# Kernel tuning notes

Hardware: AMD Instinct MI355X
Metric: run time of the kernel (lower is better)

## Reference

```python
import jax, jax.numpy as jnp
import numpy as np

T = 8          # number of adapter tasks
H = 1024       # hidden_size
I = 4096       # intermediate_size (bert dense input)
D = H // 16    # adapter bottleneck (reduction_factor=16)
B, S = 8, 512
EPS = 1e-12    # BERT LayerNorm eps


def _layernorm(x, g, b):
    mu = jnp.mean(x, axis=-1, keepdims=True)
    var = jnp.mean(jnp.square(x - mu), axis=-1, keepdims=True)
    return (x - mu) * jax.lax.rsqrt(var + EPS) * g + b


def setup_inputs() -> dict:
    key = jax.random.key(0)
    ks = jax.random.split(key, 14)
    std = 0.02
    inp = {
        "hidden_states": jax.random.normal(ks[0], (B, S, I), jnp.float32),
        "input_tensor": jax.random.normal(ks[1], (B, S, H), jnp.float32),
        "dense_w": jax.random.normal(ks[2], (H, I), jnp.float32) * std,
        "dense_b": jnp.zeros((H,), jnp.float32),
        "ln_g": jnp.ones((H,), jnp.float32),
        "ln_b": jnp.zeros((H,), jnp.float32),
        "down_w": jax.random.normal(ks[3], (T, D, H), jnp.float32) * std,
        "down_b": jnp.zeros((T, D), jnp.float32),
        "up_w": jax.random.normal(ks[4], (T, H, D), jnp.float32) * std,
        "up_b": jnp.zeros((T, H), jnp.float32),
        "key_w": jax.random.normal(ks[5], (H, H), jnp.float32) * std,
        "key_b": jnp.zeros((H,), jnp.float32),
        "query_w": jax.random.normal(ks[6], (H, H), jnp.float32) * std,
        "query_b": jnp.zeros((H,), jnp.float32),
        # value init: near-zero with identity diagonal
        "value_w": jnp.full((H, H), 1e-6, jnp.float32).at[jnp.arange(H), jnp.arange(H)].set(1.0),
    }
    return inp


def reference(hidden_states, input_tensor, dense_w, dense_b, ln_g, ln_b,
              down_w, down_b, up_w, up_b, key_w, key_b, query_w, query_b, value_w):
    # dense: [B,S,I] @ [H,I]^T -> [B,S,H]   (dropout = identity in eval)
    h = jnp.einsum('bsi,hi->bsh', hidden_states, dense_w) + dense_b
    prenorm = input_tensor + h
    adapter_in = _layernorm(prenorm, ln_g, ln_b)
    # batched per-task adapters: down-project, relu, up-project -> [T,B,S,H]
    down = jax.nn.relu(jnp.einsum('bsh,tdh->tbsd', adapter_in, down_w)
                       + down_b[:, None, None, :])
    adapter_out = jnp.einsum('tbsd,thd->tbsh', down, up_w) + up_b[:, None, None, :]
    # fusion attention over task axis T
    key = jnp.einsum('tbsh,kh->tbsk', adapter_out, key_w) + key_b
    value = jnp.einsum('tbsh,vh->tbsv', adapter_out + h[None], value_w)
    query = jnp.einsum('bsh,qh->bsq', prenorm, query_w) + query_b
    scores = jnp.sum(query[None] * key, axis=-1, keepdims=True)  # [T,B,S,1]
    probs = jax.nn.softmax(scores, axis=0)
    fusion = jnp.sum(probs * value, axis=0)                       # [B,S,H]
    return _layernorm(input_tensor + fusion, ln_g, ln_b)
```

## Files before the change

kernel.cpp:

```cpp
#include <hip/hip_runtime.h>
#include <cstdint>
#include <cstddef>

typedef float   f32x4 __attribute__((ext_vector_type(4)));
typedef _Float16 f16x8 __attribute__((ext_vector_type(8)));
typedef _Float16 f16x4 __attribute__((ext_vector_type(4)));

#define TOK  4096
#define HID  1024
#define IDIM 4096

#define GLDS16(gp, lp) __builtin_amdgcn_global_load_lds(                      \
    (const __attribute__((address_space(1))) void*)(gp),                      \
    (__attribute__((address_space(3))) void*)(lp), 16, 0, 0)


__global__ __launch_bounds__(256, 4) void gemm_dense(
    const _Float16* __restrict__ A, const _Float16* __restrict__ B,
    int K, int Kchunk, float* __restrict__ part)
{
    __shared__ _Float16 lA[2][4096];
    __shared__ _Float16 lB[2][4096];
    const int tid  = threadIdx.x;
    const int lane = tid & 63;
    const int wave = tid >> 6;
    const int m0   = blockIdx.x * 128;
    const int n0   = blockIdx.y * 128;
    const int kz0  = blockIdx.z * Kchunk;
    const int wM   = (wave & 1) * 64;
    const int wN   = (wave >> 1) * 64;

    const int srow = lane >> 2;
    const int scol = ((lane & 3) ^ ((lane >> 3) & 3)) * 8;
    const _Float16* gA0 = A + (size_t)(m0 + wave * 32 + srow) * K + kz0 + scol;
    const _Float16* gA1 = gA0 + (size_t)16 * K;
    const _Float16* gB0 = B + (size_t)(n0 + wave * 32 + srow) * K + kz0 + scol;
    const _Float16* gB1 = gB0 + (size_t)16 * K;
    const int soff = wave * 1024;

    f32x4 acc[4][4] = {};
    const int fr  = lane & 15;
    const int khr = lane >> 4;
    const int kxo = (khr ^ ((fr >> 1) & 3)) * 8;

    GLDS16(gA0, &lA[0][soff]);
    GLDS16(gA1, &lA[0][soff + 512]);
    GLDS16(gB0, &lB[0][soff]);
    GLDS16(gB1, &lB[0][soff + 512]);
    __syncthreads();

    int cur = 0;
    for (int k = 0; k < Kchunk; k += 32) {
        if (k + 32 < Kchunk) {
            const int nb = cur ^ 1;
            GLDS16(gA0 + k + 32, &lA[nb][soff]);
            GLDS16(gA1 + k + 32, &lA[nb][soff + 512]);
            GLDS16(gB0 + k + 32, &lB[nb][soff]);
            GLDS16(gB1 + k + 32, &lB[nb][soff + 512]);
        }
        f16x8 afr[4], bfr[4];
#pragma unroll
        for (int mi = 0; mi < 4; ++mi)
            afr[mi] = *(const f16x8*)(&lA[cur][(wM + mi * 16 + fr) * 32 + kxo]);
#pragma unroll
        for (int ni = 0; ni < 4; ++ni)
            bfr[ni] = *(const f16x8*)(&lB[cur][(wN + ni * 16 + fr) * 32 + kxo]);
#pragma unroll
        for (int mi = 0; mi < 4; ++mi)
#pragma unroll
            for (int ni = 0; ni < 4; ++ni)
                acc[mi][ni] = __builtin_amdgcn_mfma_f32_16x16x32_f16(
                    afr[mi], bfr[ni], acc[mi][ni], 0, 0, 0);
        __syncthreads();
        cur ^= 1;
    }

    float* dst = part + (size_t)blockIdx.z * TOK * HID;
    const int cn = lane & 15;
    const int rq = (lane >> 4) * 4;
#pragma unroll
    for (int mi = 0; mi < 4; ++mi)
#pragma unroll
        for (int r = 0; r < 4; ++r) {
            const int m = m0 + wM + mi * 16 + rq + r;
#pragma unroll
            for (int ni = 0; ni < 4; ++ni) {
                const int n = n0 + wN + ni * 16 + cn;
                dst[(size_t)m * HID + n] = acc[mi][ni][r];
            }
        }
}

template <int MODE>
__global__ __launch_bounds__(1024, 4) void gemm_w32(
    const _Float16* __restrict__ Ah, const _Float16* __restrict__ B,
    int K, int Ncols,
    float* __restrict__ outF, _Float16* __restrict__ outH,
    const float* __restrict__ bias, const float* __restrict__ addv,
    const float* __restrict__ probs, const float* __restrict__ upb,
    const _Float16* __restrict__ A2, const _Float16* __restrict__ B2,
    _Float16* __restrict__ outH2)
{
    __shared__ _Float16 lA[2][4096];
    __shared__ _Float16 lB[2][4096];
    const int tid  = threadIdx.x;
    const int lane = tid & 63;
    const int wave = tid >> 6;
    const int m0   = blockIdx.x * 128;
    int n0, half = 0;
    const _Float16* Ap = Ah;
    const _Float16* Bp = B;
    if constexpr (MODE == 5) {
        half = blockIdx.y >> 2;
        n0 = (blockIdx.y & 3) * 128;
        if (half) { Ap = A2; Bp = B2; }
    } else {
        n0 = blockIdx.y * 128;
    }
    const int wM = (wave & 3) * 32;
    const int wN = (wave >> 2) * 32;

    f32x4 acc[2][2] = {};

    const int i8   = wave & 7;
    const int srow = lane >> 2;
    const int scol = ((lane & 3) ^ ((lane >> 3) & 3)) * 8;
    const _Float16* gsrc = ((wave < 8)
        ? Ap + (size_t)(m0 + i8 * 16 + srow) * K
        : Bp + (size_t)(n0 + i8 * 16 + srow) * K) + scol;
    _Float16* ldst = ((wave < 8) ? &lA[0][0] : &lB[0][0]) + i8 * 512;

    const int fr  = lane & 15;
    const int khr = lane >> 4;
    const int kxo = (khr ^ ((fr >> 1) & 3)) * 8;

    GLDS16(gsrc, ldst);
    __syncthreads();

    int cur = 0;
    for (int k0 = 0; k0 < K; k0 += 32) {
        if (k0 + 32 < K)
            GLDS16(gsrc + k0 + 32, ldst + (cur ^ 1) * 4096);
        f16x8 afr[2], bfr[2];
#pragma unroll
        for (int mi = 0; mi < 2; ++mi)
            afr[mi] = *(const f16x8*)(&lA[cur][(wM + mi * 16 + fr) * 32 + kxo]);
#pragma unroll
        for (int ni = 0; ni < 2; ++ni)
            bfr[ni] = *(const f16x8*)(&lB[cur][(wN + ni * 16 + fr) * 32 + kxo]);
#pragma unroll
        for (int mi = 0; mi < 2; ++mi)
#pragma unroll
            for (int ni = 0; ni < 2; ++ni)
                acc[mi][ni] = __builtin_amdgcn_mfma_f32_16x16x32_f16(
                    afr[mi], bfr[ni], acc[mi][ni], 0, 0, 0);
        __syncthreads();
        cur ^= 1;
    }

    const int cn = lane & 15;
    const int rq = (lane >> 4) * 4;
#pragma unroll
    for (int mi = 0; mi < 2; ++mi)
#pragma unroll
        for (int r = 0; r < 4; ++r) {
            const int m = m0 + wM + mi * 16 + rq + r;
#pragma unroll
            for (int ni = 0; ni < 2; ++ni) {
                const int n = n0 + wN + ni * 16 + cn;
                const float v = acc[mi][ni][r];
                if constexpr (MODE == 1) {
                    const float bb = bias ? bias[n] : 0.f;
                    outH[(size_t)m * Ncols + n] = (_Float16)(v + bb);
                } else if constexpr (MODE == 3) {
                    const size_t idx = (size_t)m * Ncols + n;
                    float s = v + addv[idx];
#pragma unroll
                    for (int t = 0; t < 8; ++t)
                        s += probs[(size_t)m * 8 + t] * upb[t * 1024 + n];
                    outH[idx] = (_Float16)s;
                } else if constexpr (MODE == 4) {
                    const size_t idx = (size_t)m * Ncols + n;
                    outF[idx] = v + addv[idx];
                } else {
                    const size_t idx = (size_t)m * 512 + n;
                    if (half == 0) {
                        const float y = v + bias[n];
                        outH[idx] = (_Float16)(y > 0.f ? y : 0.f);
                    } else {
                        outH2[idx] = (_Float16)v;
                    }
                }
            }
        }
}

__global__ __launch_bounds__(256) void ln_fused(
    const float* __restrict__ part, int sk,
    const float* __restrict__ dbias, const float* __restrict__ it,
    const float* __restrict__ gam, const float* __restrict__ bet,
    float* __restrict__ h_f32, _Float16* __restrict__ ai, _Float16* __restrict__ pn)
{
    const int n = blockIdx.x, tid = threadIdx.x;
    const int lane = tid & 63, wave = tid >> 6;
    const size_t base = (size_t)n * 1024 + tid * 4;
    f32x4 h = *(const f32x4*)(dbias + tid * 4);
    for (int z = 0; z < sk; ++z)
        h += *(const f32x4*)(part + (size_t)z * TOK * HID + base);
    *(f32x4*)(h_f32 + base) = h;
    f32x4 x = h + *(const f32x4*)(it + base);
    float s = x[0] + x[1] + x[2] + x[3];
    float q = x[0] * x[0] + x[1] * x[1] + x[2] * x[2] + x[3] * x[3];
#pragma unroll
    for (int off = 1; off < 64; off <<= 1) {
        s += __shfl_xor(s, off);
        q += __shfl_xor(q, off);
    }
    __shared__ float rs[4], rq[4];
    if (lane == 0) { rs[wave] = s; rq[wave] = q; }
    __syncthreads();
    s = rs[0] + rs[1] + rs[2] + rs[3];
    q = rq[0] + rq[1] + rq[2] + rq[3];
    const float mu = s * (1.f / 1024.f);
    const float var = q * (1.f / 1024.f) - mu * mu;
    const float rstd = rsqrtf(var + 1e-12f);
    f32x4 gv = *(const f32x4*)(gam + tid * 4);
    f32x4 bv = *(const f32x4*)(bet + tid * 4);
    f16x4 av, pv;
#pragma unroll
    for (int j = 0; j < 4; ++j) {
        const float y = (x[j] - mu) * rstd * gv[j] + bv[j];
        av[j] = (_Float16)y;
        pv[j] = (_Float16)x[j];
    }
    *(f16x4*)(ai + base) = av;
    *(f16x4*)(pn + base) = pv;
}

__global__ __launch_bounds__(256) void ln_out(
    const float* __restrict__ fuse, const float* __restrict__ gam,
    const float* __restrict__ bet, float* __restrict__ outp)
{
    const int n = blockIdx.x, tid = threadIdx.x;
    const int lane = tid & 63, wave = tid >> 6;
    const size_t base = (size_t)n * 1024 + tid * 4;
    f32x4 x = *(const f32x4*)(fuse + base);
    float s = x[0] + x[1] + x[2] + x[3];
    float q = x[0] * x[0] + x[1] * x[1] + x[2] * x[2] + x[3] * x[3];
#pragma unroll
    for (int off = 1; off < 64; off <<= 1) {
        s += __shfl_xor(s, off);
        q += __shfl_xor(q, off);
    }
    __shared__ float rs[4], rq[4];
    if (lane == 0) { rs[wave] = s; rq[wave] = q; }
    __syncthreads();
    s = rs[0] + rs[1] + rs[2] + rs[3];
    q = rq[0] + rq[1] + rq[2] + rq[3];
    const float mu = s * (1.f / 1024.f);
    const float var = q * (1.f / 1024.f) - mu * mu;
    const float rstd = rsqrtf(var + 1e-12f);
    f32x4 gv = *(const f32x4*)(gam + tid * 4);
    f32x4 bv = *(const f32x4*)(bet + tid * 4);
    f32x4 y;
#pragma unroll
    for (int j = 0; j < 4; ++j) y[j] = (x[j] - mu) * rstd * gv[j] + bv[j];
    *(f32x4*)(outp + base) = y;
}

__global__ __launch_bounds__(256) void scores_softmax(
    const _Float16* __restrict__ qk, const float* __restrict__ up_b,
    const _Float16* __restrict__ down, const _Float16* __restrict__ g,
    float* __restrict__ probs_out, _Float16* __restrict__ wdown)
{
    const int n = blockIdx.x, tid = threadIdx.x;
    const int lane = tid & 63, wave = tid >> 6;
    const _Float16* qkrow = qk + (size_t)n * 1024;
    float ub[8] = {};
#pragma unroll
    for (int j = 0; j < 4; ++j) {
        const int h = tid + j * 256;
        const float qkv = (float)qkrow[h];
#pragma unroll
        for (int t = 0; t < 8; ++t) ub[t] += qkv * up_b[t * 1024 + h];
    }
#pragma unroll
    for (int off = 1; off < 64; off <<= 1) {
#pragma unroll
        for (int t = 0; t < 8; ++t) ub[t] += __shfl_xor(ub[t], off);
    }
    __shared__ float red[4][9];
    __shared__ float sd[8];
    __shared__ float pl[8];
    if (lane == 0) {
#pragma unroll
        for (int t = 0; t < 8; ++t) red[wave][t] = ub[t];
    }
    const int c0 = tid * 2;
    const size_t dbase = (size_t)n * 512;
    const float d0 = (float)down[dbase + c0];
    const float d1 = (float)down[dbase + c0 + 1];
    float pz = d0 * (float)g[dbase + c0] + d1 * (float)g[dbase + c0 + 1];
#pragma unroll
    for (int off = 1; off < 32; off <<= 1) pz += __shfl_xor(pz, off);
    if ((lane & 31) == 0) sd[wave * 2 + (lane >> 5)] = pz;
    __syncthreads();
    if (tid == 0) {
        float sc[8];
        float mx = -1e30f;
#pragma unroll
        for (int t = 0; t < 8; ++t) {
            sc[t] = sd[t] + red[0][t] + red[1][t] + red[2][t] + red[3][t];
            mx = fmaxf(mx, sc[t]);
        }
        float sum = 0.f;
#pragma unroll
        for (int t = 0; t < 8; ++t) { sc[t] = expf(sc[t] - mx); sum += sc[t]; }
        const float inv = 1.f / sum;
#pragma unroll
        for (int t = 0; t < 8; ++t) pl[t] = sc[t] * inv;
    }
    __syncthreads();
    const float pr = pl[c0 >> 6];
    wdown[dbase + c0]     = (_Float16)(pr * d0);
    wdown[dbase + c0 + 1] = (_Float16)(pr * d1);
    if (tid < 8) probs_out[(size_t)n * 8 + tid] = pl[tid];
}

__device__ inline void cvt_seg(const float* __restrict__ s, _Float16* __restrict__ d,
                               int n4, int gid, int gsz)
{
    for (int i = gid; i < n4; i += gsz) {
        f32x4 v = ((const f32x4*)s)[i];
        f16x4 o;
        o[0] = (_Float16)v[0]; o[1] = (_Float16)v[1];
        o[2] = (_Float16)v[2]; o[3] = (_Float16)v[3];
        ((f16x4*)d)[i] = o;
    }
}

__global__ __launch_bounds__(256) void convert4(
    const float* s0, _Float16* d0, int n0,
    const float* s1, _Float16* d1, int n1,
    const float* s2, _Float16* d2, int n2,
    const float* s3, _Float16* d3, int n3,
    float* bz)
{
    if (blockIdx.x == 0) {
        f32x4 z = {0.f, 0.f, 0.f, 0.f};
        *(f32x4*)(bz + threadIdx.x * 4) = z;
    }
    const int gid = blockIdx.x * 256 + threadIdx.x;
    const int gsz = gridDim.x * 256;
    cvt_seg(s0, d0, n0, gid, gsz);
    cvt_seg(s1, d1, n1, gid, gsz);
    cvt_seg(s2, d2, n2, gid, gsz);
    cvt_seg(s3, d3, n3, gid, gsz);
}

__global__ __launch_bounds__(256) void transpose_kw(
    const float* __restrict__ in, _Float16* __restrict__ outp,
    const float* __restrict__ rvec, float* __restrict__ rout)
{
    __shared__ float t[32][33];
    __shared__ float rpart[8][33];
    const int bx = blockIdx.x * 32;
    const int by = blockIdx.y * 32;
    const int tx = threadIdx.x & 31, ty = threadIdx.x >> 5;
#pragma unroll
    for (int j = 0; j < 32; j += 8)
        t[ty + j][tx] = in[(size_t)(by + ty + j) * 1024 + bx + tx];
    __syncthreads();
#pragma unroll
    for (int j = 0; j < 32; j += 8)
        outp[(size_t)(bx + ty + j) * 1024 + by + tx] = (_Float16)t[tx][ty + j];
    if (rvec) {
        float s = 0.f;
#pragma unroll
        for (int j = 0; j < 4; ++j) {
            const int k = ty * 4 + j;
            s += rvec[by + k] * t[k][tx];
        }
        rpart[ty][tx] = s;
        __syncthreads();
        if (ty == 0) {
            float v = rpart[0][tx];
#pragma unroll
            for (int r = 1; r < 8; ++r) v += rpart[r][tx];
            atomicAdd(rout + bx + tx, v);
        }
    }
}

__global__ __launch_bounds__(256) void reshape_up(
    const float* __restrict__ up_w, _Float16* __restrict__ upg,
    _Float16* __restrict__ upmix)
{
    const int i = blockIdx.x * 256 + threadIdx.x;
    const int d = i & 63;
    const int h = (i >> 6) & 1023;
    const int t = i >> 16;
    const float v = up_w[i];
    upg[(size_t)(t * 64 + d) * 1024 + h] = (_Float16)v;
    upmix[(size_t)h * 512 + t * 64 + d]  = (_Float16)v;
}

extern "C" void kernel_launch(void* const* d_in, const int* in_sizes, int n_in,
                              void* d_out, int out_size, void* d_ws, size_t ws_size,
                              hipStream_t stream)
{
    const float* hs      = (const float*)d_in[0];
    const float* it      = (const float*)d_in[1];
    const float* dense_w = (const float*)d_in[2];
    const float* dense_b = (const float*)d_in[3];
    const float* ln_g    = (const float*)d_in[4];
    const float* ln_b    = (const float*)d_in[5];
    const float* down_w  = (const float*)d_in[6];
    const float* down_b  = (const float*)d_in[7];
    const float* up_w    = (const float*)d_in[8];
    const float* up_b    = (const float*)d_in[9];
    const float* key_w   = (const float*)d_in[10];
    const float* key_b   = (const float*)d_in[11];
    const float* query_w = (const float*)d_in[12];
    const float* query_b = (const float*)d_in[13];
    const float* value_w = (const float*)d_in[14];
    float* outp = (float*)d_out;
    (void)in_sizes; (void)n_in; (void)out_size; (void)key_b;

    const size_t MiB = 1ull << 20;
    char* p = (char*)d_ws;
    _Float16* w_dense  = (_Float16*)p; p += 8 * MiB;
    _Float16* w_queryT = (_Float16*)p; p += 2 * MiB;
    _Float16* w_keyT   = (_Float16*)p; p += 2 * MiB;
    _Float16* w_value  = (_Float16*)p; p += 2 * MiB;
    _Float16* w_fuseT  = (_Float16*)p; p += 2 * MiB;
    _Float16* w_down   = (_Float16*)p; p += 1 * MiB;
    _Float16* w_upg    = (_Float16*)p; p += 1 * MiB;
    _Float16* w_upmix  = (_Float16*)p; p += 1 * MiB;
    float*    bfuse    = (float*)p;    p += 1 * MiB;
    float*    h_f32    = (float*)p;    p += 16 * MiB;
    _Float16* ai       = (_Float16*)p; p += 8 * MiB;
    _Float16* pn       = (_Float16*)p; p += 8 * MiB;
    _Float16* hs_h = (_Float16*)h_f32;
    char* rb = p;
    const int sk = (ws_size >= (size_t)(52 + 64) * MiB) ? 4 : 2;
    float*    part  = (float*)rb;
    _Float16* qk    = (_Float16*)(rb +  8 * MiB);
    _Float16* down  = (_Float16*)(rb + 16 * MiB);
    _Float16* g     = (_Float16*)(rb + 20 * MiB);
    _Float16* wdown = (_Float16*)(rb + 24 * MiB);
    float*    probs = (float*)(rb + 28 * MiB);
    float*    fuse  = (float*)rb;
    _Float16* mixed = ai;

    convert4<<<2048, 256, 0, stream>>>(hs, hs_h, TOK * IDIM / 4,
                                       dense_w, w_dense, HID * IDIM / 4,
                                       value_w, w_value, HID * HID / 4,
                                       down_w,  w_down,  512 * HID / 4,
                                       bfuse);
    transpose_kw<<<dim3(32, 32), 256, 0, stream>>>(key_w, w_keyT, query_b, bfuse);
    transpose_kw<<<dim3(32, 32), 256, 0, stream>>>(query_w, w_queryT, nullptr, nullptr);
    reshape_up<<<2048, 256, 0, stream>>>(up_w, w_upg, w_upmix);
    gemm_w32<1><<<dim3(8, 8), 1024, 0, stream>>>(
        w_keyT, w_queryT, HID, HID, nullptr, w_fuseT, nullptr, nullptr, nullptr,
        nullptr, nullptr, nullptr, nullptr);

    gemm_dense<<<dim3(32, 8, sk), 256, 0, stream>>>(hs_h, w_dense, IDIM, IDIM / sk, part);
    ln_fused<<<TOK, 256, 0, stream>>>(part, sk, dense_b, it, ln_g, ln_b, h_f32, ai, pn);
    gemm_w32<1><<<dim3(32, 8), 1024, 0, stream>>>(
        pn, w_fuseT, HID, HID, nullptr, qk, bfuse, nullptr, nullptr, nullptr,
        nullptr, nullptr, nullptr);
    gemm_w32<5><<<dim3(32, 8), 1024, 0, stream>>>(
        ai, w_down, HID, 512, nullptr, down, down_b, nullptr, nullptr, nullptr,
        qk, w_upg, g);
    scores_softmax<<<TOK, 256, 0, stream>>>(qk, up_b, down, g, probs, wdown);
    gemm_w32<3><<<dim3(32, 8), 1024, 0, stream>>>(
        wdown, w_upmix, 512, HID, nullptr, mixed, nullptr, h_f32, probs, up_b,
        nullptr, nullptr, nullptr);
    gemm_w32<4><<<dim3(32, 8), 1024, 0, stream>>>(
        mixed, w_value, HID, HID, fuse, nullptr, nullptr, it, nullptr, nullptr,
        nullptr, nullptr, nullptr);
    ln_out<<<TOK, 256, 0, stream>>>(fuse, ln_g, ln_b, outp);
}
```

Measured before the change: 345.2 us.

## Rework 128x128 GEMM tile to 4 waves with 64x64 per-wave subtiles

The secondary GEMM kernel moves from 16 waves, each computing 32x32, to 4 waves, each computing 64x64, on the same 128x128 block tile. Each wave now issues four global-to-LDS loads per stage instead of one. It also reads 4+4 fragments for 16 MFMAs, which raises the MFMA-to-LDS-read ratio and lowers barrier cost per FLOP. The MODE 3 epilogue hoists the per-row probs loads out of the column loop. The trade-off is more accumulator registers per thread and fewer waves to hide latency, since a 128x128 grid with 32x8 blocks yields only 256 blocks.

```diff
diff --git a/kernel.cpp b/kernel.cpp
--- a/kernel.cpp
+++ b/kernel.cpp
@@ -92,7 +92,7 @@
 }
 
 template <int MODE>
-__global__ __launch_bounds__(1024, 4) void gemm_w32(
+__global__ __launch_bounds__(256, 4) void gemm_tile(
     const _Float16* __restrict__ Ah, const _Float16* __restrict__ B,
     int K, int Ncols,
     float* __restrict__ outF, _Float16* __restrict__ outH,
@@ -117,41 +117,48 @@
     } else {
         n0 = blockIdx.y * 128;
     }
-    const int wM = (wave & 3) * 32;
-    const int wN = (wave >> 2) * 32;
-
-    f32x4 acc[2][2] = {};
-
-    const int i8   = wave & 7;
+    const int wM = (wave & 1) * 64;
+    const int wN = (wave >> 1) * 64;
+
     const int srow = lane >> 2;
     const int scol = ((lane & 3) ^ ((lane >> 3) & 3)) * 8;
-    const _Float16* gsrc = ((wave < 8)
-        ? Ap + (size_t)(m0 + i8 * 16 + srow) * K
-        : Bp + (size_t)(n0 + i8 * 16 + srow) * K) + scol;
-    _Float16* ldst = ((wave < 8) ? &lA[0][0] : &lB[0][0]) + i8 * 512;
-
+    const _Float16* gA0 = Ap + (size_t)(m0 + wave * 32 + srow) * K + scol;
+    const _Float16* gA1 = gA0 + (size_t)16 * K;
+    const _Float16* gB0 = Bp + (size_t)(n0 + wave * 32 + srow) * K + scol;
+    const _Float16* gB1 = gB0 + (size_t)16 * K;
+    const int soff = wave * 1024;
+
+    f32x4 acc[4][4] = {};
     const int fr  = lane & 15;
     const int khr = lane >> 4;
     const int kxo = (khr ^ ((fr >> 1) & 3)) * 8;
 
-    GLDS16(gsrc, ldst);
+    GLDS16(gA0, &lA[0][soff]);
+    GLDS16(gA1, &lA[0][soff + 512]);
+    GLDS16(gB0, &lB[0][soff]);
+    GLDS16(gB1, &lB[0][soff + 512]);
     __syncthreads();
 
     int cur = 0;
-    for (int k0 = 0; k0 < K; k0 += 32) {
-        if (k0 + 32 < K)
-            GLDS16(gsrc + k0 + 32, ldst + (cur ^ 1) * 4096);
-        f16x8 afr[2], bfr[2];
-#pragma unroll
-        for (int mi = 0; mi < 2; ++mi)
+    for (int k = 0; k < K; k += 32) {
+        if (k + 32 < K) {
+            const int nb = cur ^ 1;
+            GLDS16(gA0 + k + 32, &lA[nb][soff]);
+            GLDS16(gA1 + k + 32, &lA[nb][soff + 512]);
+            GLDS16(gB0 + k + 32, &lB[nb][soff]);
+            GLDS16(gB1 + k + 32, &lB[nb][soff + 512]);
+        }
+        f16x8 afr[4], bfr[4];
+#pragma unroll
+        for (int mi = 0; mi < 4; ++mi)
             afr[mi] = *(const f16x8*)(&lA[cur][(wM + mi * 16 + fr) * 32 + kxo]);
 #pragma unroll
-        for (int ni = 0; ni < 2; ++ni)
+        for (int ni = 0; ni < 4; ++ni)
             bfr[ni] = *(const f16x8*)(&lB[cur][(wN + ni * 16 + fr) * 32 + kxo]);
 #pragma unroll
-        for (int mi = 0; mi < 2; ++mi)
-#pragma unroll
-            for (int ni = 0; ni < 2; ++ni)
+        for (int mi = 0; mi < 4; ++mi)
+#pragma unroll
+            for (int ni = 0; ni < 4; ++ni)
                 acc[mi][ni] = __builtin_amdgcn_mfma_f32_16x16x32_f16(
                     afr[mi], bfr[ni], acc[mi][ni], 0, 0, 0);
         __syncthreads();
@@ -161,12 +168,17 @@
     const int cn = lane & 15;
     const int rq = (lane >> 4) * 4;
 #pragma unroll
-    for (int mi = 0; mi < 2; ++mi)
+    for (int mi = 0; mi < 4; ++mi)
 #pragma unroll
         for (int r = 0; r < 4; ++r) {
             const int m = m0 + wM + mi * 16 + rq + r;
-#pragma unroll
-            for (int ni = 0; ni < 2; ++ni) {
+            float pr8[8];
+            if constexpr (MODE == 3) {
+#pragma unroll
+                for (int t = 0; t < 8; ++t) pr8[t] = probs[(size_t)m * 8 + t];
+            }
+#pragma unroll
+            for (int ni = 0; ni < 4; ++ni) {
                 const int n = n0 + wN + ni * 16 + cn;
                 const float v = acc[mi][ni][r];
                 if constexpr (MODE == 1) {
@@ -177,13 +189,13 @@
                     float s = v + addv[idx];
 #pragma unroll
                     for (int t = 0; t < 8; ++t)
-                        s += probs[(size_t)m * 8 + t] * upb[t * 1024 + n];
+                        s += pr8[t] * upb[t * 1024 + n];
                     outH[idx] = (_Float16)s;
                 } else if constexpr (MODE == 4) {
                     const size_t idx = (size_t)m * Ncols + n;
                     outF[idx] = v + addv[idx];
                 } else {
-                    const size_t idx = (size_t)m * 512 + n;
+                    const size_t idx = (size_t)m * Ncols + n;
                     if (half == 0) {
                         const float y = v + bias[n];
                         outH[idx] = (_Float16)(y > 0.f ? y : 0.f);
@@ -461,23 +473,23 @@
     transpose_kw<<<dim3(32, 32), 256, 0, stream>>>(key_w, w_keyT, query_b, bfuse);
     transpose_kw<<<dim3(32, 32), 256, 0, stream>>>(query_w, w_queryT, nullptr, nullptr);
     reshape_up<<<2048, 256, 0, stream>>>(up_w, w_upg, w_upmix);
-    gemm_w32<1><<<dim3(8, 8), 1024, 0, stream>>>(
+    gemm_tile<1><<<dim3(8, 8), 256, 0, stream>>>(
         w_keyT, w_queryT, HID, HID, nullptr, w_fuseT, nullptr, nullptr, nullptr,
         nullptr, nullptr, nullptr, nullptr);
 
     gemm_dense<<<dim3(32, 8, sk), 256, 0, stream>>>(hs_h, w_dense, IDIM, IDIM / sk, part);
     ln_fused<<<TOK, 256, 0, stream>>>(part, sk, dense_b, it, ln_g, ln_b, h_f32, ai, pn);
-    gemm_w32<1><<<dim3(32, 8), 1024, 0, stream>>>(
+    gemm_tile<1><<<dim3(32, 8), 256, 0, stream>>>(
         pn, w_fuseT, HID, HID, nullptr, qk, bfuse, nullptr, nullptr, nullptr,
         nullptr, nullptr, nullptr);
-    gemm_w32<5><<<dim3(32, 8), 1024, 0, stream>>>(
+    gemm_tile<5><<<dim3(32, 8), 256, 0, stream>>>(
         ai, w_down, HID, 512, nullptr, down, down_b, nullptr, nullptr, nullptr,
         qk, w_upg, g);
     scores_softmax<<<TOK, 256, 0, stream>>>(qk, up_b, down, g, probs, wdown);
-    gemm_w32<3><<<dim3(32, 8), 1024, 0, stream>>>(
+    gemm_tile<3><<<dim3(32, 8), 256, 0, stream>>>(
         wdown, w_upmix, 512, HID, nullptr, mixed, nullptr, h_f32, probs, up_b,
         nullptr, nullptr, nullptr);
-    gemm_w32<4><<<dim3(32, 8), 1024, 0, stream>>>(
+    gemm_tile<4><<<dim3(32, 8), 256, 0, stream>>>(
         mixed, w_value, HID, HID, fuse, nullptr, nullptr, it, nullptr, nullptr,
         nullptr, nullptr, nullptr);
     ln_out<<<TOK, 256, 0, stream>>>(fuse, ln_g, ln_b, outp);
```

After: 403.4 us. 16.9% more time.

## Fold up-projection into fused query-key weight to drop per-token qk GEMM

Applied to the files above, without the earlier changes.

Precomputes the product of the up-projection weights with the combined query/key matrix, plus the bias-derived terms (WU, bg, cu), in small weight-only kernels. The second half of the mode-5 GEMM then takes pn directly against this 512x1024 matrix, so the 4096x1024x1024 qk GEMM and its intermediate buffer go away. This removes one large per-token GEMM in exchange for extra weight preprocessing on every call and an extra fp16 rounding of the combined weight product.

```diff
diff --git a/kernel.cpp b/kernel.cpp
--- a/kernel.cpp
+++ b/kernel.cpp
@@ -188,7 +188,7 @@
                         const float y = v + bias[n];
                         outH[idx] = (_Float16)(y > 0.f ? y : 0.f);
                     } else {
-                        outH2[idx] = (_Float16)v;
+                        outH2[idx] = (_Float16)(v + upb[n]);
                     }
                 }
             }
@@ -269,20 +269,21 @@
 }
 
 __global__ __launch_bounds__(256) void scores_softmax(
-    const _Float16* __restrict__ qk, const float* __restrict__ up_b,
+    const _Float16* __restrict__ pn, const float* __restrict__ WU,
+    const float* __restrict__ cu,
     const _Float16* __restrict__ down, const _Float16* __restrict__ g,
     float* __restrict__ probs_out, _Float16* __restrict__ wdown)
 {
     const int n = blockIdx.x, tid = threadIdx.x;
     const int lane = tid & 63, wave = tid >> 6;
-    const _Float16* qkrow = qk + (size_t)n * 1024;
+    const _Float16* pnrow = pn + (size_t)n * 1024;
     float ub[8] = {};
 #pragma unroll
     for (int j = 0; j < 4; ++j) {
         const int h = tid + j * 256;
-        const float qkv = (float)qkrow[h];
-#pragma unroll
-        for (int t = 0; t < 8; ++t) ub[t] += qkv * up_b[t * 1024 + h];
+        const float pv = (float)pnrow[h];
+#pragma unroll
+        for (int t = 0; t < 8; ++t) ub[t] += pv * WU[t * 1024 + h];
     }
 #pragma unroll
     for (int off = 1; off < 64; off <<= 1) {
@@ -310,7 +311,7 @@
         float mx = -1e30f;
 #pragma unroll
         for (int t = 0; t < 8; ++t) {
-            sc[t] = sd[t] + red[0][t] + red[1][t] + red[2][t] + red[3][t];
+            sc[t] = sd[t] + cu[t] + red[0][t] + red[1][t] + red[2][t] + red[3][t];
             mx = fmaxf(mx, sc[t]);
         }
         float sum = 0.f;
@@ -403,6 +404,45 @@
     const float v = up_w[i];
     upg[(size_t)(t * 64 + d) * 1024 + h] = (_Float16)v;
     upmix[(size_t)h * 512 + t * 64 + d]  = (_Float16)v;
+}
+
+__global__ __launch_bounds__(256) void make_score_weights(
+    const _Float16* __restrict__ wfuse, const _Float16* __restrict__ upg,
+    const float* __restrict__ up_b, const float* __restrict__ bfuse,
+    float* __restrict__ WU, float* __restrict__ bg, float* __restrict__ cu)
+{
+    const int b = blockIdx.x, t = threadIdx.x;
+    if (b < 4) {
+        const int h = b * 256 + t;
+        const _Float16* row = wfuse + (size_t)h * 1024;
+        float acc[8] = {};
+        for (int hp = 0; hp < 1024; hp += 8) {
+            f16x8 w = *(const f16x8*)(row + hp);
+#pragma unroll
+            for (int j = 0; j < 8; ++j) {
+                const float wv = (float)w[j];
+#pragma unroll
+                for (int tt = 0; tt < 8; ++tt)
+                    acc[tt] += wv * up_b[tt * 1024 + hp + j];
+            }
+        }
+#pragma unroll
+        for (int tt = 0; tt < 8; ++tt) WU[tt * 1024 + h] = acc[tt];
+    } else if (b < 6) {
+        const int td = (b - 4) * 256 + t;
+        const _Float16* row = upg + (size_t)td * 1024;
+        float s = 0.f;
+        for (int hp = 0; hp < 1024; hp += 8) {
+            f16x8 w = *(const f16x8*)(row + hp);
+#pragma unroll
+            for (int j = 0; j < 8; ++j) s += (float)w[j] * bfuse[hp + j];
+        }
+        bg[td] = s;
+    } else if (t < 8) {
+        float s = 0.f;
+        for (int hp = 0; hp < 1024; ++hp) s += bfuse[hp] * up_b[t * 1024 + hp];
+        cu[t] = s;
+    }
 }
 
 extern "C" void kernel_launch(void* const* d_in, const int* in_sizes, int n_in,
@@ -433,19 +473,22 @@
     _Float16* w_queryT = (_Float16*)p; p += 2 * MiB;
     _Float16* w_keyT   = (_Float16*)p; p += 2 * MiB;
     _Float16* w_value  = (_Float16*)p; p += 2 * MiB;
-    _Float16* w_fuseT  = (_Float16*)p; p += 2 * MiB;
+    _Float16* w_fuseM  = (_Float16*)p; p += 2 * MiB;
+    _Float16* w_wg     = (_Float16*)p; p += 1 * MiB;
     _Float16* w_down   = (_Float16*)p; p += 1 * MiB;
     _Float16* w_upg    = (_Float16*)p; p += 1 * MiB;
     _Float16* w_upmix  = (_Float16*)p; p += 1 * MiB;
     float*    bfuse    = (float*)p;    p += 1 * MiB;
+    float*    WU       = bfuse + 1024;
+    float*    bg       = WU + 8 * 1024;
+    float*    cu       = bg + 512;
     float*    h_f32    = (float*)p;    p += 16 * MiB;
     _Float16* ai       = (_Float16*)p; p += 8 * MiB;
     _Float16* pn       = (_Float16*)p; p += 8 * MiB;
     _Float16* hs_h = (_Float16*)h_f32;
     char* rb = p;
-    const int sk = (ws_size >= (size_t)(52 + 64) * MiB) ? 4 : 2;
+    const int sk = (ws_size >= (size_t)(53 + 64) * MiB) ? 4 : 2;
     float*    part  = (float*)rb;
-    _Float16* qk    = (_Float16*)(rb +  8 * MiB);
     _Float16* down  = (_Float16*)(rb + 16 * MiB);
     _Float16* g     = (_Float16*)(rb + 20 * MiB);
     _Float16* wdown = (_Float16*)(rb + 24 * MiB);
@@ -462,18 +505,20 @@
     transpose_kw<<<dim3(32, 32), 256, 0, stream>>>(query_w, w_queryT, nullptr, nullptr);
     reshape_up<<<2048, 256, 0, stream>>>(up_w, w_upg, w_upmix);
     gemm_w32<1><<<dim3(8, 8), 1024, 0, stream>>>(
-        w_keyT, w_queryT, HID, HID, nullptr, w_fuseT, nullptr, nullptr, nullptr,
+        w_queryT, w_keyT, HID, HID, nullptr, w_fuseM, nullptr, nullptr, nullptr,
         nullptr, nullptr, nullptr, nullptr);
+    gemm_w32<1><<<dim3(4, 8), 1024, 0, stream>>>(
+        w_upg, w_fuseM, HID, HID, nullptr, w_wg, nullptr, nullptr, nullptr,
+        nullptr, nullptr, nullptr, nullptr);
+    make_score_weights<<<7, 256, 0, stream>>>(w_fuseM, w_upg, up_b, bfuse,
+                                              WU, bg, cu);
 
     gemm_dense<<<dim3(32, 8, sk), 256, 0, stream>>>(hs_h, w_dense, IDIM, IDIM / sk, part);
     ln_fused<<<TOK, 256, 0, stream>>>(part, sk, dense_b, it, ln_g, ln_b, h_f32, ai, pn);
-    gemm_w32<1><<<dim3(32, 8), 1024, 0, stream>>>(
-        pn, w_fuseT, HID, HID, nullptr, qk, bfuse, nullptr, nullptr, nullptr,
-        nullptr, nullptr, nullptr);
     gemm_w32<5><<<dim3(32, 8), 1024, 0, stream>>>(
-        ai, w_down, HID, 512, nullptr, down, down_b, nullptr, nullptr, nullptr,
-        qk, w_upg, g);
-    scores_softmax<<<TOK, 256, 0, stream>>>(qk, up_b, down, g, probs, wdown);
+        ai, w_down, HID, 512, nullptr, down, down_b, nullptr, nullptr, bg,
+        pn, w_wg, g);
+    scores_softmax<<<TOK, 256, 0, stream>>>(pn, WU, cu, down, g, probs, wdown);
     gemm_w32<3><<<dim3(32, 8), 1024, 0, stream>>>(
         wdown, w_upmix, 512, HID, nullptr, mixed, nullptr, h_f32, probs, up_b,
         nullptr, nullptr, nullptr);
```

Result: slower. 429.4 us (+24.4%).
